# Performance work log

Measured on AMD Instinct MI355X. Metric: run time of the kernel, lower is better.

Reference implementation:

```python
import jax, jax.numpy as jnp
import numpy as np

B, N, D = 4, 1024, 1024
H, HD = 16, 64  # num_heads, head_dim


def rotate_half(x):
    x1, x2 = jnp.split(x, 2, axis=-1)
    return jnp.concatenate([-x2, x1], axis=-1)


def setup_inputs() -> dict:
    key = jax.random.key(0)
    ks = jax.random.split(key, 10)
    s = 1.0 / np.sqrt(D)
    hidden_states = jax.random.normal(ks[0], (B, N, D), jnp.float32)
    # rotary angles -> cos/sin per position per head-dim
    ang = jax.random.uniform(ks[1], (B, N, HD), jnp.float32, 0.0, 2 * np.pi)
    cos, sin = jnp.cos(ang), jnp.sin(ang)
    wq = jax.random.normal(ks[2], (D, D), jnp.float32) * s
    bq = jnp.zeros((D,), jnp.float32)
    wk = jax.random.normal(ks[3], (D, D), jnp.float32) * s  # key_bias=False
    wv = jax.random.normal(ks[4], (D, D), jnp.float32) * s
    bv = jnp.zeros((D,), jnp.float32)
    wo = jax.random.normal(ks[5], (D, D), jnp.float32) * s
    bo = jnp.zeros((D,), jnp.float32)
    return {"hidden_states": hidden_states, "cos": cos, "sin": sin,
            "wq": wq, "bq": bq, "wk": wk, "wv": wv, "bv": bv,
            "wo": wo, "bo": bo}


def reference(hidden_states, cos, sin, wq, bq, wk, wv, bv, wo, bo):
    # weights are (out, in) as in eqx Linear: y = x @ W.T + b
    q = jnp.einsum('bnd,ed->bne', hidden_states, wq) + bq
    k = jnp.einsum('bnd,ed->bne', hidden_states, wk)
    v = jnp.einsum('bnd,ed->bne', hidden_states, wv) + bv
    # [B, H, N, HD]
    q = q.reshape(B, N, H, HD).transpose(0, 2, 1, 3)
    k = k.reshape(B, N, H, HD).transpose(0, 2, 1, 3)
    v = v.reshape(B, N, H, HD).transpose(0, 2, 1, 3)
    c = cos[:, None, :, :]  # broadcast over heads
    s = sin[:, None, :, :]
    q = q * c + rotate_half(q) * s
    k = k * c + rotate_half(k) * s
    scale = 1.0 / np.sqrt(HD)
    scores = jnp.einsum('bhqd,bhkd->bhqk', q, k) * scale
    attn = jax.nn.softmax(scores, axis=-1)
    out = jnp.einsum('bhqk,bhkd->bhqd', attn, v)
    out = out.transpose(0, 2, 1, 3).reshape(B, N, D)
    return jnp.einsum('bnd,ed->bne', out, wo) + bo
```

## Files before the change

kernel.cpp:

```cpp
#include <hip/hip_runtime.h>
#include <hip/hip_bf16.h>
#include <cstdint>


typedef _Float16 half8 __attribute__((ext_vector_type(8)));
typedef _Float16 half4 __attribute__((ext_vector_type(4)));
typedef float f32x4 __attribute__((ext_vector_type(4)));

#define DEV_INLINE __device__ __forceinline__

constexpr int Bb = 4, Ns = 1024, Dd = 1024, Hh = 16, HDd = 64;
constexpr int M_ROWS = Bb * Ns;
constexpr int EQKV = 3 * Dd;

constexpr size_t OFF_HSH  = 0;
constexpr size_t SZ_HSH   = (size_t)M_ROWS * Dd * 2;
constexpr size_t OFF_WQKV = OFF_HSH + SZ_HSH;
constexpr size_t SZ_WQKV  = (size_t)EQKV * Dd * 2;
constexpr size_t OFF_WO   = OFF_WQKV + SZ_WQKV;
constexpr size_t SZ_WO    = (size_t)Dd * Dd * 2;
constexpr size_t OFF_BIAS = OFF_WO + SZ_WO;
constexpr size_t OFF_QKV  = OFF_BIAS + 16384;
constexpr size_t SZ_QKV   = (size_t)M_ROWS * EQKV * 2;
constexpr size_t OFF_QT   = OFF_QKV + SZ_QKV;
constexpr size_t SZ_HEADS = (size_t)Bb * Hh * Ns * HDd * 2;
constexpr size_t OFF_KT   = OFF_QT + SZ_HEADS;
constexpr size_t OFF_VT   = OFF_KT + SZ_HEADS;
constexpr size_t OFF_ATTN = OFF_QKV;

DEV_INLINE void async_cp16(const _Float16* g, _Float16* l) {
  __builtin_amdgcn_global_load_lds(
      (const __attribute__((address_space(1))) unsigned int*)(g),
      (__attribute__((address_space(3))) unsigned int*)(l), 16, 0, 0);
}

DEV_INLINE half4 cvt4(float4 v) {
  half4 h;
  h[0] = (_Float16)v.x; h[1] = (_Float16)v.y;
  h[2] = (_Float16)v.z; h[3] = (_Float16)v.w;
  return h;
}

__global__ __launch_bounds__(256) void cvt_kernel(
    const float* __restrict__ hs, const float* __restrict__ wq,
    const float* __restrict__ wk, const float* __restrict__ wv,
    const float* __restrict__ wo, const float* __restrict__ bq,
    const float* __restrict__ bv, _Float16* __restrict__ hsH,
    _Float16* __restrict__ wqkvH, _Float16* __restrict__ woH,
    float* __restrict__ biasP)
{
  const int gid = blockIdx.x * 256 + threadIdx.x;
  const int nHs4 = M_ROWS * Dd / 4;
  const int nW4  = 3 * Dd * Dd / 4;
  const int nWo4 = Dd * Dd / 4;
  if (gid < EQKV / 4) {
#pragma unroll
    for (int j = 0; j < 4; ++j) {
      int e = gid * 4 + j;
      biasP[e] = (e < 1024) ? bq[e] : (e < 2048 ? 0.f : bv[e - 2048]);
    }
  }
  if (gid < nHs4) {
    float4 v = reinterpret_cast<const float4*>(hs)[gid];
    reinterpret_cast<half4*>(hsH)[gid] = cvt4(v);
  } else if (gid < nHs4 + nW4) {
    int j = gid - nHs4;
    const int per = Dd * Dd / 4;
    const float* src = (j < per) ? wq : (j < 2 * per ? wk : wv);
    float4 v = reinterpret_cast<const float4*>(src)[j % per];
    reinterpret_cast<half4*>(wqkvH)[j] = cvt4(v);
  } else if (gid < nHs4 + nW4 + nWo4) {
    int j = gid - nHs4 - nW4;
    float4 v = reinterpret_cast<const float4*>(wo)[j];
    reinterpret_cast<half4*>(woH)[j] = cvt4(v);
  }
}

template<int OUTF32>
__global__ __launch_bounds__(256, 3) void gemm_bt(
    const _Float16* __restrict__ A, const _Float16* __restrict__ Bt,
    const float* __restrict__ bias, void* __restrict__ out,
    int M, int E, int K)
{
  __shared__ _Float16 As[128 * 64];
  __shared__ _Float16 Bs[128 * 64];
  const int t = threadIdx.x;
  const int lane = t & 63, wave = t >> 6;
  const int c15 = lane & 15, g = lane >> 4;
  const int wm = wave >> 1, wn = wave & 1;
  const int m0 = blockIdx.y * 128, e0 = blockIdx.x * 128;

  const int srow  = t >> 3;
  const int scol8 = ((t & 7) ^ ((t >> 3) & 7)) * 8;
  const _Float16* gA0 = A  + (size_t)(m0 + srow) * K + scol8;
  const _Float16* gB0 = Bt + (size_t)(e0 + srow) * K + scol8;
  char* lA = (char*)As + wave * 1024;
  char* lB = (char*)Bs + wave * 1024;

  const char* pA[4][2];
  const char* pB[4][2];
#pragma unroll
  for (int mi = 0; mi < 4; ++mi)
#pragma unroll
    for (int kh = 0; kh < 2; ++kh) {
      int ra = wm * 64 + mi * 16 + c15;
      pA[mi][kh] = (const char*)As + ra * 128 + (((kh * 4 + g) ^ (ra & 7)) << 4);
      int rb = wn * 64 + mi * 16 + c15;
      pB[mi][kh] = (const char*)Bs + rb * 128 + (((kh * 4 + g) ^ (rb & 7)) << 4);
    }

  f32x4 acc[4][4];
  const f32x4 zero = {0.f, 0.f, 0.f, 0.f};
#pragma unroll
  for (int i = 0; i < 4; ++i)
#pragma unroll
    for (int j = 0; j < 4; ++j) acc[i][j] = zero;

  const int nk = K >> 6;
  for (int kt = 0; kt < nk; ++kt) {
    const _Float16* ga = gA0 + kt * 64;
    const _Float16* gb = gB0 + kt * 64;
#pragma unroll
    for (int i = 0; i < 4; ++i) {
      async_cp16(ga + (size_t)(32 * i) * K, (_Float16*)(lA + i * 4096));
      async_cp16(gb + (size_t)(32 * i) * K, (_Float16*)(lB + i * 4096));
    }
    __syncthreads();
#pragma unroll
    for (int kh = 0; kh < 2; ++kh) {
      half8 a[4], b[4];
#pragma unroll
      for (int i = 0; i < 4; ++i) a[i] = *reinterpret_cast<const half8*>(pA[i][kh]);
#pragma unroll
      for (int i = 0; i < 4; ++i) b[i] = *reinterpret_cast<const half8*>(pB[i][kh]);
#pragma unroll
      for (int i = 0; i < 4; ++i)
#pragma unroll
        for (int j = 0; j < 4; ++j)
          acc[i][j] = __builtin_amdgcn_mfma_f32_16x16x32_f16(a[i], b[j], acc[i][j], 0, 0, 0);
    }
    __syncthreads();
  }

#pragma unroll
  for (int i = 0; i < 4; ++i)
#pragma unroll
    for (int j = 0; j < 4; ++j)
#pragma unroll
      for (int r = 0; r < 4; ++r) {
        int row = m0 + wm * 64 + i * 16 + g * 4 + r;
        int col = e0 + wn * 64 + j * 16 + c15;
        float v = acc[i][j][r] + bias[col];
        if (OUTF32)
          reinterpret_cast<float*>(out)[(size_t)row * E + col] = v;
        else
          reinterpret_cast<_Float16*>(out)[(size_t)row * E + col] = (_Float16)v;
      }
}

__global__ __launch_bounds__(256) void rope_kernel(
    const _Float16* __restrict__ qkvH, const float* __restrict__ cosp,
    const float* __restrict__ sinp, _Float16* __restrict__ qTo,
    _Float16* __restrict__ kTo, _Float16* __restrict__ vTo)
{
  __shared__ _Float16 Vs[64 * 72];
  const int t = threadIdx.x;
  const int bx = blockIdx.x;
  const int nt = bx & 15, bh = bx >> 4;
  const int b = bh >> 4, h = bh & 15;
  const int n0 = nt * 64;

#pragma unroll
  for (int sec = 0; sec < 2; ++sec) {
    const int basecol = sec * 1024 + h * 64;
    _Float16* dst = sec ? kTo : qTo;
#pragma unroll
    for (int ii = 0; ii < 8; ++ii) {
      int pid = t + 256 * ii;
      int r = pid >> 5, p = pid & 31;
      int n = n0 + r;
      size_t mrow = (size_t)(b * Ns + n);
      float x1 = (float)qkvH[mrow * EQKV + basecol + p];
      float x2 = (float)qkvH[mrow * EQKV + basecol + 32 + p];
      size_t cso = mrow * HDd;
      float c1 = cosp[cso + p], s1 = sinp[cso + p];
      float c2 = cosp[cso + 32 + p], s2 = sinp[cso + 32 + p];
      _Float16* o = dst + ((size_t)bh * Ns + n) * HDd;
      o[p] = (_Float16)(x1 * c1 - x2 * s1);
      o[32 + p] = (_Float16)(x2 * c2 + x1 * s2);
    }
  }
#pragma unroll
  for (int ii = 0; ii < 2; ++ii) {
    int cid = t + 256 * ii;
    int r = cid >> 3, ch = cid & 7;
    half8 v = *reinterpret_cast<const half8*>(
        qkvH + (size_t)(b * Ns + n0 + r) * EQKV + 2048 + h * 64 + ch * 8);
    *reinterpret_cast<half8*>(&Vs[r * 72 + ch * 8]) = v;
  }
  __syncthreads();
#pragma unroll
  for (int ii = 0; ii < 2; ++ii) {
    int cid = t + 256 * ii;
    int d = cid >> 3, ch = cid & 7;
    half8 w;
#pragma unroll
    for (int kk = 0; kk < 8; ++kk) w[kk] = Vs[(ch * 8 + kk) * 72 + d];
    *reinterpret_cast<half8*>(vTo + ((size_t)bh * HDd + d) * Ns + n0 + ch * 8) = w;
  }
}

__global__ __launch_bounds__(256) void attn_kernel(
    const _Float16* __restrict__ qT, const _Float16* __restrict__ kT,
    const _Float16* __restrict__ vT, _Float16* __restrict__ attnH)
{
  __shared__ _Float16 Ks[2][64 * 64];
  __shared__ _Float16 Vst[2][64 * 64];
  __shared__ _Float16 Ps[64 * 64];
  const int t = threadIdx.x;
  const int lane = t & 63, wave = t >> 6;
  const int c = lane & 15, g = lane >> 4;
  const int bx = blockIdx.x;
  const int qt = bx & 15, bh = bx >> 4;
  const int b = bh >> 4, h = bh & 15;
  const int qn0 = qt * 64;
  const int strip = wave * 16;

  const _Float16* qp = qT + ((size_t)bh * Ns + qn0 + strip + c) * HDd + g * 8;
  half8 qf0 = *reinterpret_cast<const half8*>(qp);
  half8 qf1 = *reinterpret_cast<const half8*>(qp + 32);

  half8 ones;
#pragma unroll
  for (int j = 0; j < 8; ++j) ones[j] = (_Float16)1.0f;

  f32x4 accO[4];
  f32x4 accL;
  const f32x4 zero = {0.f, 0.f, 0.f, 0.f};
#pragma unroll
  for (int d = 0; d < 4; ++d) accO[d] = zero;
  accL = zero;

  const int srow = t >> 3, sch = t & 7;
  const int ssw = (sch * 16) ^ ((srow & 7) << 4);
  const _Float16* gK = kT + ((size_t)bh * Ns + srow) * HDd + sch * 8;
  const _Float16* gV = vT + ((size_t)bh * HDd + srow) * Ns + sch * 8;
  char* wKa = (char*)Ks[0]  + srow * 128 + ssw;
  char* wVa = (char*)Vst[0] + srow * 128 + ssw;

  const char* pK[2][4];
  const char* pV[2][4];
  const half8* pP[2];
#pragma unroll
  for (int ks = 0; ks < 2; ++ks) {
#pragma unroll
    for (int i = 0; i < 4; ++i) {
      int rowk = i * 16 + c;
      pK[ks][i] = (const char*)Ks[0]  + rowk * 128 + ((ks * 64 + g * 16) ^ ((rowk & 7) << 4));
      pV[ks][i] = (const char*)Vst[0] + rowk * 128 + ((ks * 64 + g * 16) ^ ((rowk & 7) << 4));
    }
    int rowp = strip + c;
    pP[ks] = reinterpret_cast<const half8*>(
        (const char*)Ps + rowp * 128 + ((ks * 64 + g * 16) ^ ((rowp & 7) << 4)));
  }

  const float K1 = 0.18033688011112042f;
  const float K2 = -11.541560327111707f;
  char* prow = (char*)Ps + (strip + c) * 128;
  const int psw = (c & 7) << 4;

  {
    half8 k0 = *reinterpret_cast<const half8*>(gK);
    half8 k1 = *reinterpret_cast<const half8*>(gK + 32 * HDd);
    half8 v0 = *reinterpret_cast<const half8*>(gV);
    half8 v1 = *reinterpret_cast<const half8*>(gV + 32 * Ns);
    *reinterpret_cast<half8*>(wKa) = k0;
    *reinterpret_cast<half8*>(wKa + 4096) = k1;
    *reinterpret_cast<half8*>(wVa) = v0;
    *reinterpret_cast<half8*>(wVa + 4096) = v1;
  }
  __syncthreads();

  for (int jt = 0; jt < 16; ++jt) {
    const int bo = (jt & 1) * 8192;
    const bool pre = (jt + 1 < 16);
    half8 kr0, kr1, vr0, vr1;
    if (pre) {
      kr0 = *reinterpret_cast<const half8*>(gK + (jt + 1) * 4096);
      kr1 = *reinterpret_cast<const half8*>(gK + (jt + 1) * 4096 + 32 * HDd);
      vr0 = *reinterpret_cast<const half8*>(gV + (jt + 1) * 64);
      vr1 = *reinterpret_cast<const half8*>(gV + (jt + 1) * 64 + 32 * Ns);
    }

    f32x4 s[4];
#pragma unroll
    for (int i = 0; i < 4; ++i) s[i] = zero;
    __builtin_amdgcn_s_setprio(1);
#pragma unroll
    for (int i = 0; i < 4; ++i)
      s[i] = __builtin_amdgcn_mfma_f32_16x16x32_f16(
          *reinterpret_cast<const half8*>(pK[0][i] + bo), qf0, s[i], 0, 0, 0);
#pragma unroll
    for (int i = 0; i < 4; ++i)
      s[i] = __builtin_amdgcn_mfma_f32_16x16x32_f16(
          *reinterpret_cast<const half8*>(pK[1][i] + bo), qf1, s[i], 0, 0, 0);
    __builtin_amdgcn_s_setprio(0);

#pragma unroll
    for (int i = 0; i < 4; ++i) {
      half4 pk;
      pk[0] = (_Float16)__builtin_amdgcn_exp2f(fmaf(s[i][0], K1, K2));
      pk[1] = (_Float16)__builtin_amdgcn_exp2f(fmaf(s[i][1], K1, K2));
      pk[2] = (_Float16)__builtin_amdgcn_exp2f(fmaf(s[i][2], K1, K2));
      pk[3] = (_Float16)__builtin_amdgcn_exp2f(fmaf(s[i][3], K1, K2));
      *reinterpret_cast<half4*>(prow + ((i * 32 + g * 8) ^ psw)) = pk;
    }

    __builtin_amdgcn_s_setprio(1);
#pragma unroll
    for (int ks = 0; ks < 2; ++ks) {
      half8 pa = *pP[ks];
      accL = __builtin_amdgcn_mfma_f32_16x16x32_f16(pa, ones, accL, 0, 0, 0);
#pragma unroll
      for (int dt = 0; dt < 4; ++dt)
        accO[dt] = __builtin_amdgcn_mfma_f32_16x16x32_f16(
            pa, *reinterpret_cast<const half8*>(pV[ks][dt] + bo), accO[dt], 0, 0, 0);
    }
    __builtin_amdgcn_s_setprio(0);

    if (pre) {
      const int wo_ = 8192 - bo;
      *reinterpret_cast<half8*>(wKa + wo_) = kr0;
      *reinterpret_cast<half8*>(wKa + wo_ + 4096) = kr1;
      *reinterpret_cast<half8*>(wVa + wo_) = vr0;
      *reinterpret_cast<half8*>(wVa + wo_ + 4096) = vr1;
      __syncthreads();
    }
  }

#pragma unroll
  for (int r = 0; r < 4; ++r) {
    float inv = 1.f / accL[r];
    int n = qn0 + strip + g * 4 + r;
#pragma unroll
    for (int dt = 0; dt < 4; ++dt) {
      float v = accO[dt][r] * inv;
      attnH[((size_t)b * Ns + n) * Dd + h * HDd + dt * 16 + c] = (_Float16)v;
    }
  }
}

extern "C" void kernel_launch(void* const* d_in, const int* in_sizes, int n_in,
                              void* d_out, int out_size, void* d_ws, size_t ws_size,
                              hipStream_t stream) {
  const float* hs   = (const float*)d_in[0];
  const float* cosp = (const float*)d_in[1];
  const float* sinp = (const float*)d_in[2];
  const float* wq   = (const float*)d_in[3];
  const float* bq   = (const float*)d_in[4];
  const float* wk   = (const float*)d_in[5];
  const float* wv   = (const float*)d_in[6];
  const float* bv   = (const float*)d_in[7];
  const float* wo   = (const float*)d_in[8];
  const float* bo   = (const float*)d_in[9];

  char* ws = (char*)d_ws;
  _Float16* hsH   = (_Float16*)(ws + OFF_HSH);
  _Float16* wqkvH = (_Float16*)(ws + OFF_WQKV);
  _Float16* woH   = (_Float16*)(ws + OFF_WO);
  float*    biasP = (float*)(ws + OFF_BIAS);
  _Float16* qkvH  = (_Float16*)(ws + OFF_QKV);
  _Float16* qTp   = (_Float16*)(ws + OFF_QT);
  _Float16* kTp   = (_Float16*)(ws + OFF_KT);
  _Float16* vTp   = (_Float16*)(ws + OFF_VT);
  _Float16* attnH = (_Float16*)(ws + OFF_ATTN);

  cvt_kernel<<<8192, 256, 0, stream>>>(hs, wq, wk, wv, wo, bq, bv,
                                       hsH, wqkvH, woH, biasP);
  gemm_bt<0><<<dim3(EQKV / 128, M_ROWS / 128), 256, 0, stream>>>(
      hsH, wqkvH, biasP, qkvH, M_ROWS, EQKV, Dd);
  rope_kernel<<<Bb * Hh * (Ns / 64), 256, 0, stream>>>(qkvH, cosp, sinp,
                                                       qTp, kTp, vTp);
  attn_kernel<<<Bb * Hh * (Ns / 64), 256, 0, stream>>>(qTp, kTp, vTp, attnH);
  gemm_bt<1><<<dim3(Dd / 128, M_ROWS / 128), 256, 0, stream>>>(
      attnH, woH, bo, d_out, M_ROWS, Dd, Dd);
}
```

Measured before the change: 109.2 us.

## Software-pipeline attention loop: overlap QK of tile j with PV of tile j-1

Restructures the attention inner loop so each iteration computes QK^T and softmax for the current key tile while doing the P·V product for the previous tile. P is double-buffered in LDS, and the V load schedule is shifted by one tile, with an epilogue for the last PV step. The aim is to let exp work and MFMA chains from independent tiles interleave and to remove a serial dependency within an iteration. It adds 8KB of LDS, which could reduce occupancy, and the loop now synchronises on every iteration, including the last.

```diff
diff --git a/kernel.cpp b/kernel.cpp
--- a/kernel.cpp
+++ b/kernel.cpp
@@ -216,7 +216,7 @@
 {
   __shared__ _Float16 Ks[2][64 * 64];
   __shared__ _Float16 Vst[2][64 * 64];
-  __shared__ _Float16 Ps[64 * 64];
+  __shared__ _Float16 Ps[2][64 * 64];
   const int t = threadIdx.x;
   const int lane = t & 63, wave = t >> 6;
   const int c = lane & 15, g = lane >> 4;
@@ -250,7 +250,7 @@
 
   const char* pK[2][4];
   const char* pV[2][4];
-  const half8* pP[2];
+  const char* pP[2];
 #pragma unroll
   for (int ks = 0; ks < 2; ++ks) {
 #pragma unroll
@@ -260,37 +260,34 @@
       pV[ks][i] = (const char*)Vst[0] + rowk * 128 + ((ks * 64 + g * 16) ^ ((rowk & 7) << 4));
     }
     int rowp = strip + c;
-    pP[ks] = reinterpret_cast<const half8*>(
-        (const char*)Ps + rowp * 128 + ((ks * 64 + g * 16) ^ ((rowp & 7) << 4)));
+    pP[ks] = (const char*)Ps[0] + rowp * 128 + ((ks * 64 + g * 16) ^ ((rowp & 7) << 4));
   }
 
   const float K1 = 0.18033688011112042f;
   const float K2 = -11.541560327111707f;
-  char* prow = (char*)Ps + (strip + c) * 128;
+  char* prow = (char*)Ps[0] + (strip + c) * 128;
   const int psw = (c & 7) << 4;
 
   {
     half8 k0 = *reinterpret_cast<const half8*>(gK);
     half8 k1 = *reinterpret_cast<const half8*>(gK + 32 * HDd);
-    half8 v0 = *reinterpret_cast<const half8*>(gV);
-    half8 v1 = *reinterpret_cast<const half8*>(gV + 32 * Ns);
     *reinterpret_cast<half8*>(wKa) = k0;
     *reinterpret_cast<half8*>(wKa + 4096) = k1;
-    *reinterpret_cast<half8*>(wVa) = v0;
-    *reinterpret_cast<half8*>(wVa + 4096) = v1;
   }
   __syncthreads();
 
   for (int jt = 0; jt < 16; ++jt) {
-    const int bo = (jt & 1) * 8192;
-    const bool pre = (jt + 1 < 16);
+    const int bo  = (jt & 1) * 8192;
+    const int ro  = 8192 - bo;
+    const bool haveK = (jt + 1 < 16);
+
     half8 kr0, kr1, vr0, vr1;
-    if (pre) {
+    if (haveK) {
       kr0 = *reinterpret_cast<const half8*>(gK + (jt + 1) * 4096);
       kr1 = *reinterpret_cast<const half8*>(gK + (jt + 1) * 4096 + 32 * HDd);
-      vr0 = *reinterpret_cast<const half8*>(gV + (jt + 1) * 64);
-      vr1 = *reinterpret_cast<const half8*>(gV + (jt + 1) * 64 + 32 * Ns);
-    }
+    }
+    vr0 = *reinterpret_cast<const half8*>(gV + jt * 64);
+    vr1 = *reinterpret_cast<const half8*>(gV + jt * 64 + 32 * Ns);
 
     f32x4 s[4];
 #pragma unroll
@@ -313,29 +310,45 @@
       pk[1] = (_Float16)__builtin_amdgcn_exp2f(fmaf(s[i][1], K1, K2));
       pk[2] = (_Float16)__builtin_amdgcn_exp2f(fmaf(s[i][2], K1, K2));
       pk[3] = (_Float16)__builtin_amdgcn_exp2f(fmaf(s[i][3], K1, K2));
-      *reinterpret_cast<half4*>(prow + ((i * 32 + g * 8) ^ psw)) = pk;
-    }
-
+      *reinterpret_cast<half4*>(prow + bo + ((i * 32 + g * 8) ^ psw)) = pk;
+    }
+
+    if (jt > 0) {
+      __builtin_amdgcn_s_setprio(1);
+#pragma unroll
+      for (int ks = 0; ks < 2; ++ks) {
+        half8 pa = *reinterpret_cast<const half8*>(pP[ks] + ro);
+        accL = __builtin_amdgcn_mfma_f32_16x16x32_f16(pa, ones, accL, 0, 0, 0);
+#pragma unroll
+        for (int dt = 0; dt < 4; ++dt)
+          accO[dt] = __builtin_amdgcn_mfma_f32_16x16x32_f16(
+              pa, *reinterpret_cast<const half8*>(pV[ks][dt] + ro), accO[dt], 0, 0, 0);
+      }
+      __builtin_amdgcn_s_setprio(0);
+    }
+
+    if (haveK) {
+      *reinterpret_cast<half8*>(wKa + ro) = kr0;
+      *reinterpret_cast<half8*>(wKa + ro + 4096) = kr1;
+    }
+    *reinterpret_cast<half8*>(wVa + bo) = vr0;
+    *reinterpret_cast<half8*>(wVa + bo + 4096) = vr1;
+    __syncthreads();
+  }
+
+  {
+    const int ro = 8192;
     __builtin_amdgcn_s_setprio(1);
 #pragma unroll
     for (int ks = 0; ks < 2; ++ks) {
-      half8 pa = *pP[ks];
+      half8 pa = *reinterpret_cast<const half8*>(pP[ks] + ro);
       accL = __builtin_amdgcn_mfma_f32_16x16x32_f16(pa, ones, accL, 0, 0, 0);
 #pragma unroll
       for (int dt = 0; dt < 4; ++dt)
         accO[dt] = __builtin_amdgcn_mfma_f32_16x16x32_f16(
-            pa, *reinterpret_cast<const half8*>(pV[ks][dt] + bo), accO[dt], 0, 0, 0);
+            pa, *reinterpret_cast<const half8*>(pV[ks][dt] + ro), accO[dt], 0, 0, 0);
     }
     __builtin_amdgcn_s_setprio(0);
-
-    if (pre) {
-      const int wo_ = 8192 - bo;
-      *reinterpret_cast<half8*>(wKa + wo_) = kr0;
-      *reinterpret_cast<half8*>(wKa + wo_ + 4096) = kr1;
-      *reinterpret_cast<half8*>(wVa + wo_) = vr0;
-      *reinterpret_cast<half8*>(wVa + wo_ + 4096) = vr1;
-      __syncthreads();
-    }
   }
 
 #pragma unroll
```

After: 113.3 us. +3.7%, slower.

## Fuse RoPE and head-major scatter into QKV GEMM epilogue

Applied to the files above, without the earlier changes.

The QKV projection GEMM epilogue now applies the rotary embedding to Q and K directly and writes them in head-major layout, and writes V head-major into a smaller buffer. The standalone rope kernel is reduced to a V transpose. This removes the full fp16 QKV intermediate round trip through memory and the separate rope pass. The epilogue now does scattered 2-byte stores and cos/sin loads per element, which may be less coalesced than before.

```diff
diff --git a/kernel.cpp b/kernel.cpp
--- a/kernel.cpp
+++ b/kernel.cpp
@@ -20,13 +20,12 @@
 constexpr size_t OFF_WO   = OFF_WQKV + SZ_WQKV;
 constexpr size_t SZ_WO    = (size_t)Dd * Dd * 2;
 constexpr size_t OFF_BIAS = OFF_WO + SZ_WO;
-constexpr size_t OFF_QKV  = OFF_BIAS + 16384;
-constexpr size_t SZ_QKV   = (size_t)M_ROWS * EQKV * 2;
-constexpr size_t OFF_QT   = OFF_QKV + SZ_QKV;
+constexpr size_t OFF_VR   = OFF_BIAS + 16384;
 constexpr size_t SZ_HEADS = (size_t)Bb * Hh * Ns * HDd * 2;
+constexpr size_t OFF_QT   = OFF_VR + SZ_HEADS;
 constexpr size_t OFF_KT   = OFF_QT + SZ_HEADS;
 constexpr size_t OFF_VT   = OFF_KT + SZ_HEADS;
-constexpr size_t OFF_ATTN = OFF_QKV;
+constexpr size_t OFF_ATTN = OFF_VR;
 
 DEV_INLINE void async_cp16(const _Float16* g, _Float16* l) {
   __builtin_amdgcn_global_load_lds(
@@ -76,10 +75,12 @@
   }
 }
 
-template<int OUTF32>
+template<int MODE>
 __global__ __launch_bounds__(256, 3) void gemm_bt(
     const _Float16* __restrict__ A, const _Float16* __restrict__ Bt,
     const float* __restrict__ bias, void* __restrict__ out,
+    const float* __restrict__ cosp, const float* __restrict__ sinp,
+    _Float16* __restrict__ qT, _Float16* __restrict__ kT,
     int M, int E, int K)
 {
   __shared__ _Float16 As[128 * 64];
@@ -142,60 +143,77 @@
     __syncthreads();
   }
 
-#pragma unroll
-  for (int i = 0; i < 4; ++i)
-#pragma unroll
-    for (int j = 0; j < 4; ++j)
-#pragma unroll
-      for (int r = 0; r < 4; ++r) {
-        int row = m0 + wm * 64 + i * 16 + g * 4 + r;
-        int col = e0 + wn * 64 + j * 16 + c15;
-        float v = acc[i][j][r] + bias[col];
-        if (OUTF32)
-          reinterpret_cast<float*>(out)[(size_t)row * E + col] = v;
-        else
-          reinterpret_cast<_Float16*>(out)[(size_t)row * E + col] = (_Float16)v;
-      }
-}
-
-__global__ __launch_bounds__(256) void rope_kernel(
-    const _Float16* __restrict__ qkvH, const float* __restrict__ cosp,
-    const float* __restrict__ sinp, _Float16* __restrict__ qTo,
-    _Float16* __restrict__ kTo, _Float16* __restrict__ vTo)
+  if (MODE == 1) {
+#pragma unroll
+    for (int i = 0; i < 4; ++i)
+#pragma unroll
+      for (int j = 0; j < 4; ++j)
+#pragma unroll
+        for (int r = 0; r < 4; ++r) {
+          int row = m0 + wm * 64 + i * 16 + g * 4 + r;
+          int col = e0 + wn * 64 + j * 16 + c15;
+          reinterpret_cast<float*>(out)[(size_t)row * E + col] =
+              acc[i][j][r] + bias[col];
+        }
+  } else {
+    const int scol = e0 + wn * 64;
+    const int sec = scol >> 10;
+    const int h = (scol & 1023) >> 6;
+    if (sec < 2) {
+      _Float16* dst = sec ? kT : qT;
+#pragma unroll
+      for (int i = 0; i < 4; ++i)
+#pragma unroll
+        for (int r = 0; r < 4; ++r) {
+          int row = m0 + wm * 64 + i * 16 + g * 4 + r;
+          int bh = (row >> 10) * Hh + h;
+          size_t obase = ((size_t)bh * Ns + (row & 1023)) * HDd;
+          const float* cb = cosp + (size_t)row * HDd;
+          const float* sb = sinp + (size_t)row * HDd;
+#pragma unroll
+          for (int j = 0; j < 2; ++j) {
+            int hd = j * 16 + c15;
+            float x1 = acc[i][j][r]     + bias[scol + hd];
+            float x2 = acc[i][j + 2][r] + bias[scol + hd + 32];
+            float c1 = cb[hd],      s1 = sb[hd];
+            float c2 = cb[hd + 32], s2 = sb[hd + 32];
+            dst[obase + hd]      = (_Float16)(x1 * c1 - x2 * s1);
+            dst[obase + hd + 32] = (_Float16)(x2 * c2 + x1 * s2);
+          }
+        }
+    } else {
+      _Float16* vR = (_Float16*)out;
+#pragma unroll
+      for (int i = 0; i < 4; ++i)
+#pragma unroll
+        for (int r = 0; r < 4; ++r) {
+          int row = m0 + wm * 64 + i * 16 + g * 4 + r;
+          int bh = (row >> 10) * Hh + h;
+          size_t obase = ((size_t)bh * Ns + (row & 1023)) * HDd;
+#pragma unroll
+          for (int j = 0; j < 4; ++j) {
+            int hd = j * 16 + c15;
+            vR[obase + hd] = (_Float16)(acc[i][j][r] + bias[scol + hd]);
+          }
+        }
+    }
+  }
+}
+
+__global__ __launch_bounds__(256) void vtrans_kernel(
+    const _Float16* __restrict__ vR, _Float16* __restrict__ vTo)
 {
   __shared__ _Float16 Vs[64 * 72];
   const int t = threadIdx.x;
   const int bx = blockIdx.x;
   const int nt = bx & 15, bh = bx >> 4;
-  const int b = bh >> 4, h = bh & 15;
   const int n0 = nt * 64;
-
-#pragma unroll
-  for (int sec = 0; sec < 2; ++sec) {
-    const int basecol = sec * 1024 + h * 64;
-    _Float16* dst = sec ? kTo : qTo;
-#pragma unroll
-    for (int ii = 0; ii < 8; ++ii) {
-      int pid = t + 256 * ii;
-      int r = pid >> 5, p = pid & 31;
-      int n = n0 + r;
-      size_t mrow = (size_t)(b * Ns + n);
-      float x1 = (float)qkvH[mrow * EQKV + basecol + p];
-      float x2 = (float)qkvH[mrow * EQKV + basecol + 32 + p];
-      size_t cso = mrow * HDd;
-      float c1 = cosp[cso + p], s1 = sinp[cso + p];
-      float c2 = cosp[cso + 32 + p], s2 = sinp[cso + 32 + p];
-      _Float16* o = dst + ((size_t)bh * Ns + n) * HDd;
-      o[p] = (_Float16)(x1 * c1 - x2 * s1);
-      o[32 + p] = (_Float16)(x2 * c2 + x1 * s2);
-    }
-  }
 #pragma unroll
   for (int ii = 0; ii < 2; ++ii) {
     int cid = t + 256 * ii;
     int r = cid >> 3, ch = cid & 7;
     half8 v = *reinterpret_cast<const half8*>(
-        qkvH + (size_t)(b * Ns + n0 + r) * EQKV + 2048 + h * 64 + ch * 8);
+        vR + ((size_t)bh * Ns + n0 + r) * HDd + ch * 8);
     *reinterpret_cast<half8*>(&Vs[r * 72 + ch * 8]) = v;
   }
   __syncthreads();
@@ -369,7 +387,7 @@
   _Float16* wqkvH = (_Float16*)(ws + OFF_WQKV);
   _Float16* woH   = (_Float16*)(ws + OFF_WO);
   float*    biasP = (float*)(ws + OFF_BIAS);
-  _Float16* qkvH  = (_Float16*)(ws + OFF_QKV);
+  _Float16* vRp   = (_Float16*)(ws + OFF_VR);
   _Float16* qTp   = (_Float16*)(ws + OFF_QT);
   _Float16* kTp   = (_Float16*)(ws + OFF_KT);
   _Float16* vTp   = (_Float16*)(ws + OFF_VT);
@@ -378,10 +396,10 @@
   cvt_kernel<<<8192, 256, 0, stream>>>(hs, wq, wk, wv, wo, bq, bv,
                                        hsH, wqkvH, woH, biasP);
   gemm_bt<0><<<dim3(EQKV / 128, M_ROWS / 128), 256, 0, stream>>>(
-      hsH, wqkvH, biasP, qkvH, M_ROWS, EQKV, Dd);
-  rope_kernel<<<Bb * Hh * (Ns / 64), 256, 0, stream>>>(qkvH, cosp, sinp,
-                                                       qTp, kTp, vTp);
+      hsH, wqkvH, biasP, vRp, cosp, sinp, qTp, kTp, M_ROWS, EQKV, Dd);
+  vtrans_kernel<<<Bb * Hh * (Ns / 64), 256, 0, stream>>>(vRp, vTp);
   attn_kernel<<<Bb * Hh * (Ns / 64), 256, 0, stream>>>(qTp, kTp, vTp, attnH);
   gemm_bt<1><<<dim3(Dd / 128, M_ROWS / 128), 256, 0, stream>>>(
-      attnH, woH, bo, d_out, M_ROWS, Dd, Dd);
-}
+      attnH, woH, bo, d_out, nullptr, nullptr, nullptr, nullptr,
+      M_ROWS, Dd, Dd);
+}
```

After: 105.8 us. 3.1% less time.
